# Performance work log

Measured on AMD Instinct MI355X. Metric: run time of the kernel, lower is better.

## Reference

```python
import jax, jax.numpy as jnp
import numpy as np

EMB, HID = 256, 516
VX, VY = 32000, 32000
SRC, TGT, B = 64, 65, 32


def _lstm_cell(xt, h, c, Wih, Whh, b):
    # PyTorch gate order: i, f, g, o
    gates = xt @ Wih.T + h @ Whh.T + b  # [B, 4H]
    i, f, g, o = jnp.split(gates, 4, axis=-1)
    c = jax.nn.sigmoid(f) * c + jax.nn.sigmoid(i) * jnp.tanh(g)
    h = jax.nn.sigmoid(o) * jnp.tanh(c)
    return h, c


def setup_inputs() -> dict:
    key = jax.random.key(0)
    ks = jax.random.split(key, 32)
    s = 0.05
    n = lambda k, shp: (jax.random.normal(k, shp, jnp.float32) * s)
    inp = {
        "x": jax.random.randint(ks[0], (SRC, B), 0, VX),
        "y": jax.random.randint(ks[1], (TGT, B), 0, VY),
        "encemb": n(ks[2], (VX, EMB)),
        "decemb": n(ks[3], (VX, EMB)),  # sized from vocab_x, as in original
        "enc_Wih0": n(ks[4], (4 * HID, EMB)),
        "enc_Whh0": n(ks[5], (4 * HID, HID)),
        "enc_bih0": n(ks[6], (4 * HID,)),
        "enc_bhh0": n(ks[7], (4 * HID,)),
        "enc_Wih1": n(ks[8], (4 * HID, HID)),
        "enc_Whh1": n(ks[9], (4 * HID, HID)),
        "enc_bih1": n(ks[10], (4 * HID,)),
        "enc_bhh1": n(ks[11], (4 * HID,)),
        "dec_Wih0": n(ks[12], (4 * HID, EMB)),
        "dec_Whh0": n(ks[13], (4 * HID, HID)),
        "dec_bih0": n(ks[14], (4 * HID,)),
        "dec_bhh0": n(ks[15], (4 * HID,)),
        "dec_Wih1": n(ks[16], (4 * HID, HID)),
        "dec_Whh1": n(ks[17], (4 * HID, HID)),
        "dec_bih1": n(ks[18], (4 * HID,)),
        "dec_bhh1": n(ks[19], (4 * HID,)),
        "Wout": n(ks[20], (VY, HID)),
        "bout": n(ks[21], (VY,)),
    }
    return inp


def reference(x, y, encemb, decemb,
              enc_Wih0, enc_Whh0, enc_bih0, enc_bhh0,
              enc_Wih1, enc_Whh1, enc_bih1, enc_bhh1,
              dec_Wih0, dec_Whh0, dec_bih0, dec_bhh0,
              dec_Wih1, dec_Whh1, dec_bih1, dec_bhh1,
              Wout, bout):
    Bn = x.shape[1]
    z = jnp.zeros((Bn, HID), jnp.float32)
    be0 = enc_bih0 + enc_bhh0
    be1 = enc_bih1 + enc_bhh1
    bd0 = dec_bih0 + dec_bhh0
    bd1 = dec_bih1 + dec_bhh1

    # ---- encoder: 2-layer LSTM over embedded source (dropout = identity/eval) ----
    e_x = encemb[x]  # [S, B, E]

    def enc_step(carry, xt):
        h0, c0, h1, c1 = carry
        h0, c0 = _lstm_cell(xt, h0, c0, enc_Wih0, enc_Whh0, be0)
        h1, c1 = _lstm_cell(h0, h1, c1, enc_Wih1, enc_Whh1, be1)
        return (h0, c0, h1, c1), None

    carry, _ = jax.lax.scan(enc_step, (z, z, z, z), e_x)

    # ---- decoder: per-step teacher-forced decode + summed per-step mean CE ----
    def dec_step(carry, ys):
        yt, ytn = ys  # current token [B], next token [B]
        h0, c0, h1, c1 = carry
        xt = decemb[yt]  # [B, E]
        h0, c0 = _lstm_cell(xt, h0, c0, dec_Wih0, dec_Whh0, bd0)
        h1, c1 = _lstm_cell(h0, h1, c1, dec_Wih1, dec_Whh1, bd1)
        logits = h1 @ Wout.T + bout  # [B, V]
        logp = jax.nn.log_softmax(logits, axis=-1)
        step_loss = -jnp.mean(jnp.take_along_axis(logp, ytn[:, None], axis=1))
        return (h0, c0, h1, c1), step_loss

    _, losses = jax.lax.scan(dec_step, carry, (y[:-1], y[1:]))
    return jnp.sum(losses)
```

## Files before the change

kernel.cpp:

```cpp
#include <hip/hip_runtime.h>

typedef __attribute__((ext_vector_type(8))) short short8;
typedef __attribute__((ext_vector_type(4))) float f32x4;
typedef __attribute__((ext_vector_type(4))) unsigned u32x4;
typedef unsigned long long ull;

constexpr int H    = 516;
constexpr int GP   = 2080;
constexpr int KH   = 544;
constexpr int KE   = 256;
constexpr int NB   = 65;
constexpr int SB   = 32;
constexpr int SEQ  = 64;
constexpr int MROW = 2048;
constexpr int V    = 32000;
constexpr int NBN  = 250;

__device__ __forceinline__ float bf2f(short s) {
  unsigned u = ((unsigned)(unsigned short)s) << 16;
  float f; __builtin_memcpy(&f, &u, 4); return f;
}
__device__ __forceinline__ short f2bf(float f) {
  unsigned u; __builtin_memcpy(&u, &f, 4);
  u += 0x7fffu + ((u >> 16) & 1u);
  return (short)(u >> 16);
}
__device__ __forceinline__ float sigm(float x){ return 1.f/(1.f+__expf(-x)); }
__device__ __forceinline__ float tanh_(float x){ float e=__expf(-2.f*x); return (1.f-e)/(1.f+e); }

__global__ void k_pack_gates(const float* __restrict__ W1, const float* __restrict__ W2,
                             short* __restrict__ dst, int ksteps) {
  int gid = blockIdx.x * 256 + threadIdx.x;
  int total = NB * 2 * ksteps * 64;
  if (gid >= total) return;
  int lane = gid & 63;
  int rest = gid >> 6;
  int ks = rest % ksteps; rest /= ksteps;
  int nt = rest & 1; int bid = rest >> 1;
  int chat = bid * 32 + nt * 16 + (lane & 15);
  int u = chat >> 2, g = chat & 3;
  int kb = ks * 32 + (lane >> 4) * 8;
  short8 v;
#pragma unroll
  for (int j = 0; j < 8; ++j) {
    int k = kb + j;
    const float* src = W1; int kk = k;
    if (k >= KH) { src = W2; kk = k - KH; }
    float f = 0.f;
    if (u < H && kk < H) f = src[(size_t)(g * H + u) * H + kk];
    v[j] = f2bf(f);
  }
  *(short8*)(dst + (size_t)gid * 8) = v;
}

__global__ void k_pack_wout(const float* __restrict__ Wout, short* __restrict__ dst) {
  int gid = blockIdx.x * 256 + threadIdx.x;
  if (gid >= V * (KH / 8)) return;
  int row = gid / (KH / 8);
  int kb = (gid % (KH / 8)) * 8;
  short8 v;
#pragma unroll
  for (int j = 0; j < 8; ++j) {
    int k = kb + j;
    v[j] = f2bf(k < H ? Wout[(size_t)row * H + k] : 0.f);
  }
  *(short8*)(dst + (size_t)gid * 8) = v;
}

__global__ void k_pack_wih(const float* __restrict__ Wih0, short* __restrict__ dst) {
  int gid = blockIdx.x * 256 + threadIdx.x;
  if (gid >= GP * (KE / 8)) return;
  int chat = gid / (KE / 8);
  int kb = (gid % (KE / 8)) * 8;
  int u = chat >> 2, g = chat & 3;
  short8 v;
#pragma unroll
  for (int j = 0; j < 8; ++j)
    v[j] = f2bf(u < H ? Wih0[(size_t)(g * H + u) * KE + kb + j] : 0.f);
  *(short8*)(dst + (size_t)gid * 8) = v;
}

__global__ void k_pack_bias(const float* ebih0, const float* ebhh0, const float* ebih1, const float* ebhh1,
                            const float* dbih0, const float* dbhh0, const float* dbih1, const float* dbhh1,
                            float* b0e, float* b1e, float* b0d, float* b1d) {
  int chat = blockIdx.x * 256 + threadIdx.x;
  if (chat >= GP) return;
  int u = chat >> 2, g = chat & 3, n = g * H + u;
  bool ok = (u < H);
  b0e[chat] = ok ? ebih0[n] + ebhh0[n] : 0.f;
  b1e[chat] = ok ? ebih1[n] + ebhh1[n] : 0.f;
  b0d[chat] = ok ? dbih0[n] + dbhh0[n] : 0.f;
  b1d[chat] = ok ? dbih1[n] + dbhh1[n] : 0.f;
}

__global__ void __launch_bounds__(256) k_embproj(const short* __restrict__ WihP,
                                                 const float* __restrict__ emb,
                                                 const int* __restrict__ toks,
                                                 const float* __restrict__ b0P,
                                                 float* __restrict__ X0P) {
  int tid = threadIdx.x, w = tid >> 6, lane = tid & 63, q = lane >> 4, col = lane & 15;
  int mt = blockIdx.x;
  int ntile = blockIdx.y * 4 + w;
  int tb = ntile * 16 + col;
  int tok = toks[tb];
  const short* Ap = WihP + (size_t)(mt * 16 + col) * KE + q * 8;
  const float* Bp = emb + (size_t)tok * KE + q * 8;
  f32x4 acc = {0.f, 0.f, 0.f, 0.f};
#pragma unroll
  for (int ks = 0; ks < 8; ++ks) {
    short8 a = *(const short8*)(Ap + ks * 32);
    const f32x4* b4 = (const f32x4*)(Bp + ks * 32);
    f32x4 b0v = b4[0], b1v = b4[1];
    short8 bb;
    bb[0]=f2bf(b0v[0]); bb[1]=f2bf(b0v[1]); bb[2]=f2bf(b0v[2]); bb[3]=f2bf(b0v[3]);
    bb[4]=f2bf(b1v[0]); bb[5]=f2bf(b1v[1]); bb[6]=f2bf(b1v[2]); bb[7]=f2bf(b1v[3]);
    acc = __builtin_amdgcn_mfma_f32_16x16x32_bf16(a, bb, acc, 0, 0, 0);
  }
  int chat0 = mt * 16 + q * 4;
  f32x4 bias = *(const f32x4*)(b0P + chat0);
  int t = tb >> 5, b = tb & 31;
  float* dst = X0P + ((size_t)t * GP) * 32 + b;
#pragma unroll
  for (int r = 0; r < 4; ++r)
    dst[(size_t)(chat0 + r) * 32] = acc[r] + bias[r];
}

#define WL(dst, addr) asm volatile("global_load_dwordx4 %0, %1, off" : "=&v"(dst) : "v"(addr))
#define SW0 do { __builtin_amdgcn_s_waitcnt(0x0F70); __builtin_amdgcn_sched_barrier(0); } while (0)

template <int N>
__device__ __forceinline__ void vmwait() {
  __builtin_amdgcn_s_waitcnt((N & 15) | (0x7 << 4) | (0xF << 8) | ((N >> 4) << 14));
  __builtin_amdgcn_sched_barrier(0);
}

template <int NPT, int NP1, int P>
__device__ __forceinline__ void phase1(short8 (&fA)[NPT], short8 (&fB)[NPT], const short8 (&wr)[28],
                                       f32x4& p00, f32x4& p01, f32x4& p10, f32x4& p11,
                                       f32x4& q00, f32x4& q01, f32x4& q10, f32x4& q11) {
  if constexpr (P < NP1) {
    vmwait<2 * (NPT - 1 - P)>();
    p00 = __builtin_amdgcn_mfma_f32_16x16x32_bf16(fA[P], wr[4*P+0], p00, 0, 0, 0);
    p01 = __builtin_amdgcn_mfma_f32_16x16x32_bf16(fA[P], wr[4*P+1], p01, 0, 0, 0);
    p10 = __builtin_amdgcn_mfma_f32_16x16x32_bf16(fB[P], wr[4*P+0], p10, 0, 0, 0);
    p11 = __builtin_amdgcn_mfma_f32_16x16x32_bf16(fB[P], wr[4*P+1], p11, 0, 0, 0);
    q00 = __builtin_amdgcn_mfma_f32_16x16x32_bf16(fA[P], wr[4*P+2], q00, 0, 0, 0);
    q01 = __builtin_amdgcn_mfma_f32_16x16x32_bf16(fA[P], wr[4*P+3], q01, 0, 0, 0);
    q10 = __builtin_amdgcn_mfma_f32_16x16x32_bf16(fB[P], wr[4*P+2], q10, 0, 0, 0);
    q11 = __builtin_amdgcn_mfma_f32_16x16x32_bf16(fB[P], wr[4*P+3], q11, 0, 0, 0);
    phase1<NPT, NP1, P + 1>(fA, fB, wr, p00, p01, p10, p11, q00, q01, q10, q11);
  }
}

template <int NPT, int NP1, int P>
__device__ __forceinline__ void phase2(short8 (&fA)[NPT], short8 (&fB)[NPT], const short8 (&wr)[28],
                                       f32x4& q00, f32x4& q01, f32x4& q10, f32x4& q11) {
  if constexpr (NP1 + P < NPT) {
    vmwait<2 * (NPT - NP1 - 1 - P)>();
    q00 = __builtin_amdgcn_mfma_f32_16x16x32_bf16(fA[NP1+P], wr[4*NP1 + 2*P + 0], q00, 0, 0, 0);
    q01 = __builtin_amdgcn_mfma_f32_16x16x32_bf16(fA[NP1+P], wr[4*NP1 + 2*P + 1], q01, 0, 0, 0);
    q10 = __builtin_amdgcn_mfma_f32_16x16x32_bf16(fB[NP1+P], wr[4*NP1 + 2*P + 0], q10, 0, 0, 0);
    q11 = __builtin_amdgcn_mfma_f32_16x16x32_bf16(fB[NP1+P], wr[4*NP1 + 2*P + 1], q11, 0, 0, 0);
    phase2<NPT, NP1, P + 1>(fA, fB, wr, q00, q01, q10, q11);
  }
}

template <int NPT, int NP1>
__device__ __forceinline__ void run_gemm(u32x4 sr1, int sb1, u32x4 sr2, int sb2, int voff,
                                         const short8 (&wr)[28],
                                         f32x4& p00, f32x4& p01, f32x4& p10, f32x4& p11,
                                         f32x4& q00, f32x4& q01, f32x4& q10, f32x4& q11) {
  short8 fA[NPT], fB[NPT];
#pragma unroll
  for (int p = 0; p < NP1; ++p)
    asm volatile("buffer_load_dwordx4 %0, %2, %3, %4 offen sc0 sc1\n\t"
                 "buffer_load_dwordx4 %1, %2, %3, %4 offen offset:256 sc0 sc1"
                 : "=&v"(fA[p]), "=&v"(fB[p])
                 : "v"(voff), "s"(sr1), "s"(sb1 + p * 2048));
#pragma unroll
  for (int p = NP1; p < NPT; ++p)
    asm volatile("buffer_load_dwordx4 %0, %2, %3, %4 offen sc0 sc1\n\t"
                 "buffer_load_dwordx4 %1, %2, %3, %4 offen offset:256 sc0 sc1"
                 : "=&v"(fA[p]), "=&v"(fB[p])
                 : "v"(voff), "s"(sr2), "s"(sb2 + (p - NP1) * 2048));
  phase1<NPT, NP1, 0>(fA, fB, wr, p00, p01, p10, p11, q00, q01, q10, q11);
  phase2<NPT, NP1, 0>(fA, fB, wr, q00, q01, q10, q11);
}

struct RecArgs {
  const short *WAe, *WBe, *WAd, *WBd;
  const float *X0e, *X0d, *b1e, *b1d;
  short *hst, *H1P;
  unsigned *bar;
};

__global__ void __launch_bounds__(256, 1) k_recur(RecArgs A) {
  const int tid = threadIdx.x, lane = tid & 63, w = tid >> 6;
  const int q = lane >> 4, col = lane & 15;
  const int bid = blockIdx.x;
  __shared__ float g0a[32][33], g0b[32][33], g0c[32][33];
  __shared__ float g1a[32][33], g1b[32][33], g1c[32][33], g1d[32][33];
  __shared__ float c0[32][8], c1[32][8];
  const int tl = tid & 127, cb = tl >> 2, up = tl & 3;
  if (tid < 128) { c0[cb][up * 2] = 0.f; c0[cb][up * 2 + 1] = 0.f; }
  else           { c1[cb][up * 2] = 0.f; c1[cb][up * 2 + 1] = 0.f; }

  float (*gp0)[33] = (w == 0) ? g0a : (w == 1) ? g0b : g0c;
  float (*gp1)[33] = (w == 0) ? g1a : (w == 1) ? g1b : (w == 2) ? g1c : g1d;

  const int voff = q * 512 + col * 16;
  short8 wr[28];
  float b1r[8];

  for (int i = 0; i <= 128; ++i) {
    const int rp = (i + 1) & 1, wp = i & 1;

    if (i == 0 || i == 64) {
      const short* wa = ((i == 64) ? A.WAd : A.WAe) + (size_t)bid * 17408 + lane * 8;
      if (w == 0) {
#pragma unroll
        for (int j = 0; j < 6; ++j) { WL(wr[4*j], wa + j*512); WL(wr[4*j+1], wa + 8704 + j*512); }
      } else if (w == 1) {
#pragma unroll
        for (int j = 0; j < 7; ++j) { WL(wr[4*j], wa + (6+j)*512); WL(wr[4*j+1], wa + 8704 + (6+j)*512); }
      } else if (w == 2) {
#pragma unroll
        for (int j = 0; j < 4; ++j) { WL(wr[4*j], wa + (13+j)*512); WL(wr[4*j+1], wa + 8704 + (13+j)*512); }
      }
      SW0;
    }
    if (i == 0 || i == 65) {
      const short* wb = ((i == 65) ? A.WBd : A.WBe) + (size_t)bid * 34816 + lane * 8;
      if (w == 0) {
#pragma unroll
        for (int j = 0; j < 6; ++j) { WL(wr[4*j+2], wb + j*512); WL(wr[4*j+3], wb + 17408 + j*512); }
      } else if (w == 1) {
#pragma unroll
        for (int j = 0; j < 7; ++j) { WL(wr[4*j+2], wb + (6+j)*512); WL(wr[4*j+3], wb + 17408 + (6+j)*512); }
      } else if (w == 2) {
#pragma unroll
        for (int j = 0; j < 4; ++j) { WL(wr[4*j+2], wb + (13+j)*512); WL(wr[4*j+3], wb + 17408 + (13+j)*512); }
#pragma unroll
        for (int j = 0; j < 5; ++j) { WL(wr[16+2*j], wb + (17+j)*512); WL(wr[16+2*j+1], wb + 17408 + (17+j)*512); }
      } else {
#pragma unroll
        for (int j = 0; j < 12; ++j) { WL(wr[2*j], wb + (22+j)*512); WL(wr[2*j+1], wb + 17408 + (22+j)*512); }
      }
      SW0;
      if (tid >= 128) {
        const float* b1p = (i == 65) ? A.b1d : A.b1e;
#pragma unroll
        for (int j = 0; j < 8; ++j) b1r[j] = b1p[bid * 32 + up * 8 + j];
      }
    }

    float x0r[8];
    if (tid < 128) {
      const float* X0 = (i >> 6) ? A.X0d : A.X0e;
      const float* xp = X0 + ((size_t)(i & 63) * GP + bid * 32 + up * 8) * 32 + cb;
#pragma unroll
      for (int j = 0; j < 8; ++j) x0r[j] = xp[j * 32];
    }

    ull ba = (ull)(size_t)A.hst + (size_t)rp * 69632u;
    u32x4 sr0 = {(unsigned)ba, (unsigned)(ba >> 32), 0xffffffffu, 0x00020000u};
    ull bb2 = ba + 34816u;
    u32x4 sr1 = {(unsigned)bb2, (unsigned)(bb2 >> 32), 0xffffffffu, 0x00020000u};

    f32x4 p00 = {0.f,0.f,0.f,0.f}, p01 = p00, p10 = p00, p11 = p00;
    f32x4 q00 = p00, q01 = p00, q10 = p00, q11 = p00;
    if (w == 0)      run_gemm<6, 6>(sr0, 0,     sr0, 0,     voff, wr, p00,p01,p10,p11, q00,q01,q10,q11);
    else if (w == 1) run_gemm<7, 7>(sr0, 12288, sr0, 0,     voff, wr, p00,p01,p10,p11, q00,q01,q10,q11);
    else if (w == 2) run_gemm<9, 4>(sr0, 26624, sr1, 0,     voff, wr, p00,p01,p10,p11, q00,q01,q10,q11);
    else             run_gemm<12, 0>(sr0, 0,    sr1, 10240, voff, wr, p00,p01,p10,p11, q00,q01,q10,q11);

#pragma unroll
    for (int r = 0; r < 4; ++r) {
      if (w < 3) {
        gp0[q * 4 + r][col] = p00[r];      gp0[q * 4 + r][16 + col] = p01[r];
        gp0[16 + q * 4 + r][col] = p10[r]; gp0[16 + q * 4 + r][16 + col] = p11[r];
      }
      gp1[q * 4 + r][col] = q00[r];      gp1[q * 4 + r][16 + col] = q01[r];
      gp1[16 + q * 4 + r][col] = q10[r]; gp1[16 + q * 4 + r][16 + col] = q11[r];
    }
    __syncthreads();

    if (tid < 128) {
      if (i < 128) {
        unsigned hv = 0;
#pragma unroll
        for (int s = 0; s < 2; ++s) {
          int base = up * 8 + s * 4;
          float gi = g0a[cb][base+0] + g0b[cb][base+0] + g0c[cb][base+0] + x0r[s*4+0];
          float gf = g0a[cb][base+1] + g0b[cb][base+1] + g0c[cb][base+1] + x0r[s*4+1];
          float gg = g0a[cb][base+2] + g0b[cb][base+2] + g0c[cb][base+2] + x0r[s*4+2];
          float go = g0a[cb][base+3] + g0b[cb][base+3] + g0c[cb][base+3] + x0r[s*4+3];
          float c = c0[cb][up * 2 + s];
          float cn = sigm(gf) * c + sigm(gi) * tanh_(gg);
          float hn = sigm(go) * tanh_(cn);
          c0[cb][up * 2 + s] = cn;
          hv |= ((unsigned)(unsigned short)f2bf(hn)) << (16 * s);
        }
        __hip_atomic_store((unsigned*)A.hst + wp * 17408 + bid * 128 + cb * 4 + up, hv,
                           __ATOMIC_RELAXED, __HIP_MEMORY_SCOPE_AGENT);
      }
    } else {
      if (i >= 1) {
        const int i1 = i - 1;
        unsigned hv = 0;
#pragma unroll
        for (int s = 0; s < 2; ++s) {
          int base = up * 8 + s * 4;
          float gi = g1a[cb][base+0] + g1b[cb][base+0] + g1c[cb][base+0] + g1d[cb][base+0] + b1r[s*4+0];
          float gf = g1a[cb][base+1] + g1b[cb][base+1] + g1c[cb][base+1] + g1d[cb][base+1] + b1r[s*4+1];
          float gg = g1a[cb][base+2] + g1b[cb][base+2] + g1c[cb][base+2] + g1d[cb][base+2] + b1r[s*4+2];
          float go = g1a[cb][base+3] + g1b[cb][base+3] + g1c[cb][base+3] + g1d[cb][base+3] + b1r[s*4+3];
          float c = c1[cb][up * 2 + s];
          float cn = sigm(gf) * c + sigm(gi) * tanh_(gg);
          float hn = sigm(go) * tanh_(cn);
          c1[cb][up * 2 + s] = cn;
          hv |= ((unsigned)(unsigned short)f2bf(hn)) << (16 * s);
        }
        __hip_atomic_store((unsigned*)A.hst + wp * 17408 + 8704 + bid * 128 + cb * 4 + up, hv,
                           __ATOMIC_RELAXED, __HIP_MEMORY_SCOPE_AGENT);
        if (i1 >= 64)
          *((unsigned*)A.H1P + (size_t)((i1 - 64) * SB + cb) * 272 + bid * 4 + up) = hv;
      }
    }

    if (i < 128) {
      asm volatile("s_waitcnt vmcnt(0)" ::: "memory");
      __syncthreads();
      if (tid == 0)
        __hip_atomic_store(A.bar + bid * 16, (unsigned)(i + 1),
                           __ATOMIC_RELAXED, __HIP_MEMORY_SCOPE_AGENT);
      if (tid < 64) {
        const unsigned tgt = (unsigned)(i + 1);
        unsigned* f1 = A.bar + lane * 16;
        unsigned* f2 = A.bar + (lane + 1) * 16;
        while (true) {
          unsigned a = __hip_atomic_load(f1, __ATOMIC_RELAXED, __HIP_MEMORY_SCOPE_AGENT);
          unsigned b = __hip_atomic_load(f2, __ATOMIC_RELAXED, __HIP_MEMORY_SCOPE_AGENT);
          if (__all((a >= tgt) && (b >= tgt))) break;
        }
      }
      __syncthreads();
    }
  }
}

__global__ void __launch_bounds__(256) k_project(const short* __restrict__ H1P,
                                                 const short* __restrict__ WoutP,
                                                 const float* __restrict__ bout,
                                                 float* __restrict__ partials) {
  int bM = blockIdx.x, bN = blockIdx.y;
  int tid = threadIdx.x, w = tid >> 6, lane = tid & 63, q = lane >> 4, col = lane & 15;
  int wm = w >> 1, wn = w & 1;
  __shared__ __align__(16) short As[128 * 32];
  __shared__ __align__(16) short Bs[128 * 32];
  __shared__ float sred[128][2];
  f32x4 acc[4][4];
#pragma unroll
  for (int mi = 0; mi < 4; ++mi)
#pragma unroll
    for (int ni = 0; ni < 4; ++ni) acc[mi][ni] = (f32x4){0.f, 0.f, 0.f, 0.f};

  for (int ks = 0; ks < 17; ++ks) {
#pragma unroll
    for (int i = 0; i < 2; ++i) {
      int chunk = tid * 2 + i;
      int row = chunk >> 2, ch = chunk & 3;
      ((short8*)As)[chunk] = *(const short8*)(H1P  + (size_t)(bM * 128 + row) * KH + ks * 32 + ch * 8);
      ((short8*)Bs)[chunk] = *(const short8*)(WoutP + (size_t)(bN * 128 + row) * KH + ks * 32 + ch * 8);
    }
    __syncthreads();
    short8 af[4], bf[4];
#pragma unroll
    for (int mi = 0; mi < 4; ++mi) af[mi] = *(const short8*)(As + (wm * 64 + mi * 16 + col) * 32 + q * 8);
#pragma unroll
    for (int ni = 0; ni < 4; ++ni) bf[ni] = *(const short8*)(Bs + (wn * 64 + ni * 16 + col) * 32 + q * 8);
#pragma unroll
    for (int mi = 0; mi < 4; ++mi)
#pragma unroll
      for (int ni = 0; ni < 4; ++ni)
        acc[mi][ni] = __builtin_amdgcn_mfma_f32_16x16x32_bf16(af[mi], bf[ni], acc[mi][ni], 0, 0, 0);
    __syncthreads();
  }
  float bias[4];
#pragma unroll
  for (int ni = 0; ni < 4; ++ni) bias[ni] = bout[bN * 128 + wn * 64 + ni * 16 + col];
#pragma unroll
  for (int mi = 0; mi < 4; ++mi) {
#pragma unroll
    for (int r = 0; r < 4; ++r) {
      float s = 0.f;
#pragma unroll
      for (int ni = 0; ni < 4; ++ni) s += __expf(acc[mi][ni][r] + bias[ni]);
      s += __shfl_xor(s, 1, 64); s += __shfl_xor(s, 2, 64);
      s += __shfl_xor(s, 4, 64); s += __shfl_xor(s, 8, 64);
      if (col == 0) sred[wm * 64 + mi * 16 + q * 4 + r][wn] = s;
    }
  }
  __syncthreads();
  if (tid < 128)
    partials[(size_t)(bM * 128 + tid) * NBN + bN] = sred[tid][0] + sred[tid][1];
}

__global__ void __launch_bounds__(256) k_finish(const float* __restrict__ partials,
                                                const short* __restrict__ H1P,
                                                const float* __restrict__ Wout,
                                                const float* __restrict__ bout,
                                                const int* __restrict__ y,
                                                float* __restrict__ out) {
  int tid = threadIdx.x, w = tid >> 6, lane = tid & 63;
  int row = blockIdx.x * 4 + w;
  float s = 0.f;
  for (int j = lane; j < NBN; j += 64) s += partials[(size_t)row * NBN + j];
#pragma unroll
  for (int off = 32; off > 0; off >>= 1) s += __shfl_down(s, off, 64);
  int tok = y[row + 32];
  float d = 0.f;
  for (int k = lane; k < H; k += 64)
    d += bf2f(H1P[(size_t)row * KH + k]) * Wout[(size_t)tok * H + k];
#pragma unroll
  for (int off = 32; off > 0; off >>= 1) d += __shfl_down(d, off, 64);
  __shared__ float bsum[4];
  if (lane == 0) bsum[w] = __logf(s) - (d + bout[tok]);
  __syncthreads();
  if (tid == 0) atomicAdd(out, (bsum[0] + bsum[1] + bsum[2] + bsum[3]) * (1.f / 32.f));
}

extern "C" void kernel_launch(void* const* d_in, const int* in_sizes, int n_in,
                              void* d_out, int out_size, void* d_ws, size_t ws_size,
                              hipStream_t stream) {
  const int*   x      = (const int*)d_in[0];
  const int*   y      = (const int*)d_in[1];
  const float* encemb = (const float*)d_in[2];
  const float* decemb = (const float*)d_in[3];
  const float* eWih0  = (const float*)d_in[4];
  const float* eWhh0  = (const float*)d_in[5];
  const float* ebih0  = (const float*)d_in[6];
  const float* ebhh0  = (const float*)d_in[7];
  const float* eWih1  = (const float*)d_in[8];
  const float* eWhh1  = (const float*)d_in[9];
  const float* ebih1  = (const float*)d_in[10];
  const float* ebhh1  = (const float*)d_in[11];
  const float* dWih0  = (const float*)d_in[12];
  const float* dWhh0  = (const float*)d_in[13];
  const float* dbih0  = (const float*)d_in[14];
  const float* dbhh0  = (const float*)d_in[15];
  const float* dWih1  = (const float*)d_in[16];
  const float* dWhh1  = (const float*)d_in[17];
  const float* dbih1  = (const float*)d_in[18];
  const float* dbhh1  = (const float*)d_in[19];
  const float* Wout   = (const float*)d_in[20];
  const float* bout   = (const float*)d_in[21];
  float* out = (float*)d_out;

  char* wsb = (char*)d_ws;
  size_t off = 0;
  auto alloc = [&](size_t bytes) -> void* {
    void* p = wsb + off;
    off += (bytes + 255) & ~(size_t)255;
    return p;
  };
  short* WoutP = (short*)alloc((size_t)V * KH * 2);
  short* WAe   = (short*)alloc((size_t)NB * 17408 * 2);
  short* WBe   = (short*)alloc((size_t)NB * 34816 * 2);
  short* WAd   = (short*)alloc((size_t)NB * 17408 * 2);
  short* WBd   = (short*)alloc((size_t)NB * 34816 * 2);
  short* WihPe = (short*)alloc((size_t)GP * KE * 2);
  short* WihPd = (short*)alloc((size_t)GP * KE * 2);
  float* b0e   = (float*)alloc(GP * 4);
  float* b1e   = (float*)alloc(GP * 4);
  float* b0d   = (float*)alloc(GP * 4);
  float* b1d   = (float*)alloc(GP * 4);
  float* X0e   = (float*)alloc((size_t)SEQ * GP * SB * 4);
  float* X0d   = (float*)alloc((size_t)SEQ * GP * SB * 4);
  short* hst   = (short*)alloc((size_t)2 * 69632);
  short* H1P   = (short*)alloc((size_t)MROW * KH * 2);
  float* parts = (float*)alloc((size_t)MROW * NBN * 4);
  unsigned* bar = (unsigned*)alloc(NB * 64);

  hipMemsetAsync(d_out, 0, sizeof(float), stream);
  hipMemsetAsync(hst, 0, (size_t)2 * 69632, stream);
  hipMemsetAsync(bar, 0, NB * 64, stream);

  k_pack_bias<<<(GP + 255) / 256, 256, 0, stream>>>(ebih0, ebhh0, ebih1, ebhh1,
                                                    dbih0, dbhh0, dbih1, dbhh1,
                                                    b0e, b1e, b0d, b1d);
  k_pack_wih<<<(GP * KE / 8 + 255) / 256, 256, 0, stream>>>(eWih0, WihPe);
  k_pack_wih<<<(GP * KE / 8 + 255) / 256, 256, 0, stream>>>(dWih0, WihPd);
  {
    int totA = NB * 2 * 17 * 64, totB = NB * 2 * 34 * 64;
    k_pack_gates<<<(totA + 255) / 256, 256, 0, stream>>>(eWhh0, eWhh0, WAe, 17);
    k_pack_gates<<<(totB + 255) / 256, 256, 0, stream>>>(eWih1, eWhh1, WBe, 34);
    k_pack_gates<<<(totA + 255) / 256, 256, 0, stream>>>(dWhh0, dWhh0, WAd, 17);
    k_pack_gates<<<(totB + 255) / 256, 256, 0, stream>>>(dWih1, dWhh1, WBd, 34);
  }
  k_pack_wout<<<(V * (KH / 8) + 255) / 256, 256, 0, stream>>>(Wout, WoutP);

  k_embproj<<<dim3(GP / 16, 32), 256, 0, stream>>>(WihPe, encemb, x, b0e, X0e);
  k_embproj<<<dim3(GP / 16, 32), 256, 0, stream>>>(WihPd, decemb, y, b0d, X0d);

  RecArgs ra{WAe, WBe, WAd, WBd, X0e, X0d, b1e, b1d, hst, H1P, bar};
  void* kargs[] = {&ra};
  hipLaunchCooperativeKernel((const void*)k_recur, dim3(NB), dim3(256), kargs, 0, stream);

  k_project<<<dim3(MROW / 128, NBN), 256, 0, stream>>>(H1P, WoutP, bout, parts);
  k_finish<<<MROW / 4, 256, 0, stream>>>(parts, H1P, Wout, bout, y, out);
}
```

Measured before the change: 961.1 us.

## Enlarge projection GEMM tiles to 256x256 with register prefetch and padded LDS

The vocabulary projection kernel moves from 128x128 tiles with 4 waves to 256x256 tiles with 8 waves, each wave computing 128x64. The next K-slice is prefetched into registers while MFMAs run, and LDS rows are padded to 36 shorts to reduce bank conflicts. Larger tiles cut global reloads of H1P and Wout and halve the partials width. The cost is a grid of only 1000 blocks at one block per CU and higher register pressure.

```diff
diff --git a/kernel.cpp b/kernel.cpp
--- a/kernel.cpp
+++ b/kernel.cpp
@@ -14,7 +14,7 @@
 constexpr int SEQ  = 64;
 constexpr int MROW = 2048;
 constexpr int V    = 32000;
-constexpr int NBN  = 250;
+constexpr int NBN  = 125;
 
 __device__ __forceinline__ float bf2f(short s) {
   unsigned u = ((unsigned)(unsigned short)s) << 16;
@@ -349,48 +349,72 @@
   }
 }
 
-__global__ void __launch_bounds__(256) k_project(const short* __restrict__ H1P,
-                                                 const short* __restrict__ WoutP,
-                                                 const float* __restrict__ bout,
-                                                 float* __restrict__ partials) {
-  int bM = blockIdx.x, bN = blockIdx.y;
-  int tid = threadIdx.x, w = tid >> 6, lane = tid & 63, q = lane >> 4, col = lane & 15;
-  int wm = w >> 1, wn = w & 1;
-  __shared__ __align__(16) short As[128 * 32];
-  __shared__ __align__(16) short Bs[128 * 32];
-  __shared__ float sred[128][2];
-  f32x4 acc[4][4];
-#pragma unroll
-  for (int mi = 0; mi < 4; ++mi)
+__global__ void __launch_bounds__(512, 1) k_project(const short* __restrict__ H1P,
+                                                    const short* __restrict__ WoutP,
+                                                    const float* __restrict__ bout,
+                                                    float* __restrict__ partials) {
+  const int bM = blockIdx.x, bN = blockIdx.y;
+  const int tid = threadIdx.x, w = tid >> 6, lane = tid & 63, q = lane >> 4, col = lane & 15;
+  const int wm = w >> 2, wn = w & 3;
+  __shared__ __align__(16) short As[256 * 36];
+  __shared__ __align__(16) short Bs[256 * 36];
+  __shared__ float sred[256][4];
+  f32x4 acc[8][4];
+#pragma unroll
+  for (int mi = 0; mi < 8; ++mi)
 #pragma unroll
     for (int ni = 0; ni < 4; ++ni) acc[mi][ni] = (f32x4){0.f, 0.f, 0.f, 0.f};
 
+  int rowi[2], chi[2];
+#pragma unroll
+  for (int i = 0; i < 2; ++i) { int c = tid * 2 + i; rowi[i] = c >> 2; chi[i] = c & 3; }
+  const short* srcA0 = H1P  + (size_t)(bM * 256) * KH;
+  const short* srcB0 = WoutP + (size_t)(bN * 256) * KH;
+
+  short8 ra[2], rb[2];
+#pragma unroll
+  for (int i = 0; i < 2; ++i) {
+    ra[i] = *(const short8*)(srcA0 + (size_t)rowi[i] * KH + chi[i] * 8);
+    rb[i] = *(const short8*)(srcB0 + (size_t)rowi[i] * KH + chi[i] * 8);
+  }
+
   for (int ks = 0; ks < 17; ++ks) {
 #pragma unroll
     for (int i = 0; i < 2; ++i) {
-      int chunk = tid * 2 + i;
-      int row = chunk >> 2, ch = chunk & 3;
-      ((short8*)As)[chunk] = *(const short8*)(H1P  + (size_t)(bM * 128 + row) * KH + ks * 32 + ch * 8);
-      ((short8*)Bs)[chunk] = *(const short8*)(WoutP + (size_t)(bN * 128 + row) * KH + ks * 32 + ch * 8);
+      *(short8*)(As + rowi[i] * 36 + chi[i] * 8) = ra[i];
+      *(short8*)(Bs + rowi[i] * 36 + chi[i] * 8) = rb[i];
     }
     __syncthreads();
-    short8 af[4], bf[4];
-#pragma unroll
-    for (int mi = 0; mi < 4; ++mi) af[mi] = *(const short8*)(As + (wm * 64 + mi * 16 + col) * 32 + q * 8);
-#pragma unroll
-    for (int ni = 0; ni < 4; ++ni) bf[ni] = *(const short8*)(Bs + (wn * 64 + ni * 16 + col) * 32 + q * 8);
-#pragma unroll
-    for (int mi = 0; mi < 4; ++mi)
+    short8 na[2], nb[2];
+    if (ks < 16) {
+#pragma unroll
+      for (int i = 0; i < 2; ++i) {
+        na[i] = *(const short8*)(srcA0 + (size_t)rowi[i] * KH + (ks + 1) * 32 + chi[i] * 8);
+        nb[i] = *(const short8*)(srcB0 + (size_t)rowi[i] * KH + (ks + 1) * 32 + chi[i] * 8);
+      }
+    }
+    short8 af[8], bf[4];
+#pragma unroll
+    for (int mi = 0; mi < 8; ++mi)
+      af[mi] = *(const short8*)(As + (wm * 128 + mi * 16 + col) * 36 + q * 8);
+#pragma unroll
+    for (int ni = 0; ni < 4; ++ni)
+      bf[ni] = *(const short8*)(Bs + (wn * 64 + ni * 16 + col) * 36 + q * 8);
+#pragma unroll
+    for (int mi = 0; mi < 8; ++mi)
 #pragma unroll
       for (int ni = 0; ni < 4; ++ni)
         acc[mi][ni] = __builtin_amdgcn_mfma_f32_16x16x32_bf16(af[mi], bf[ni], acc[mi][ni], 0, 0, 0);
     __syncthreads();
-  }
+#pragma unroll
+    for (int i = 0; i < 2; ++i) { ra[i] = na[i]; rb[i] = nb[i]; }
+  }
+
   float bias[4];
 #pragma unroll
-  for (int ni = 0; ni < 4; ++ni) bias[ni] = bout[bN * 128 + wn * 64 + ni * 16 + col];
-#pragma unroll
-  for (int mi = 0; mi < 4; ++mi) {
+  for (int ni = 0; ni < 4; ++ni) bias[ni] = bout[bN * 256 + wn * 64 + ni * 16 + col];
+#pragma unroll
+  for (int mi = 0; mi < 8; ++mi) {
 #pragma unroll
     for (int r = 0; r < 4; ++r) {
       float s = 0.f;
@@ -398,12 +422,13 @@
       for (int ni = 0; ni < 4; ++ni) s += __expf(acc[mi][ni][r] + bias[ni]);
       s += __shfl_xor(s, 1, 64); s += __shfl_xor(s, 2, 64);
       s += __shfl_xor(s, 4, 64); s += __shfl_xor(s, 8, 64);
-      if (col == 0) sred[wm * 64 + mi * 16 + q * 4 + r][wn] = s;
+      if (col == 0) sred[wm * 128 + mi * 16 + q * 4 + r][wn] = s;
     }
   }
   __syncthreads();
-  if (tid < 128)
-    partials[(size_t)(bM * 128 + tid) * NBN + bN] = sred[tid][0] + sred[tid][1];
+  if (tid < 256)
+    partials[(size_t)(bM * 256 + tid) * NBN + bN] =
+        sred[tid][0] + sred[tid][1] + sred[tid][2] + sred[tid][3];
 }
 
 __global__ void __launch_bounds__(256) k_finish(const float* __restrict__ partials,
@@ -507,6 +532,6 @@
   void* kargs[] = {&ra};
   hipLaunchCooperativeKernel((const void*)k_recur, dim3(NB), dim3(256), kargs, 0, stream);
 
-  k_project<<<dim3(MROW / 128, NBN), 256, 0, stream>>>(H1P, WoutP, bout, parts);
+  k_project<<<dim3(MROW / 256, NBN), 512, 0, stream>>>(H1P, WoutP, bout, parts);
   k_finish<<<MROW / 4, 256, 0, stream>>>(parts, H1P, Wout, bout, y, out);
 }
```

Result: no change. 979.6 us (+1.9%).
